# Optimization experiments

Measured on AMD Instinct MI355X. Metric: run time of the kernel, lower is better.

## Reference

```python
import jax, jax.numpy as jnp
import numpy as np
from jax import lax


def extract_patches(x, kh, kw, sh, sw):
    # x: [B,H,W,C] -> [B,oh,ow,kh,kw,C], same element order as tf.image.extract_patches
    B, H, W, C = x.shape
    oh = (H - kh) // sh + 1
    ow = (W - kw) // sw + 1
    rows = jnp.arange(oh)[:, None] * sh + jnp.arange(kh)[None, :]  # [oh,kh]
    cols = jnp.arange(ow)[:, None] * sw + jnp.arange(kw)[None, :]  # [ow,kw]
    p = x[:, rows]            # [B,oh,kh,W,C]
    p = p[:, :, :, cols]      # [B,oh,kh,ow,kw,C]
    return jnp.transpose(p, (0, 1, 3, 2, 4, 5))  # [B,oh,ow,kh,kw,C]


def fastgrnn(x, W, U, bg, bu, zeta, nu):
    # FastGRNN: z=sigmoid(Wx+Uh+bg); c=tanh(Wx+Uh+bu); h'=z*h+(sig(zeta)*(1-z)+sig(nu))*c
    # x: [N,T,D] -> final hidden [N,H]
    wx = jnp.einsum('ntd,dh->nth', x, W)  # precompute input projection
    z_gate = jax.nn.sigmoid(zeta)
    n_gate = jax.nn.sigmoid(nu)

    def step(h, wx_t):
        pre = wx_t + h @ U
        z = jax.nn.sigmoid(pre + bg)
        c = jnp.tanh(pre + bu)
        h_new = z * h + (z_gate * (1.0 - z) + n_gate) * c
        return h_new, None

    h0 = jnp.zeros((x.shape[0], W.shape[1]), x.dtype)
    hT, _ = lax.scan(step, h0, jnp.swapaxes(wx, 0, 1))  # scan over T
    return hT


def rnnpool_forward(inputs, W1, U1, bg1, bu1, zeta1, nu1,
                    W2, U2, bg2, bu2, zeta2, nu2, kh, kw, sh, sw):
    B, H, Wd, C = inputs.shape
    oh = (H - kh) // sh + 1
    ow = (Wd - kw) // sw + 1
    patches = extract_patches(inputs, kh, kw, sh, sw)          # [B,oh,ow,kh,kw,C]
    N = B * oh * ow
    p = patches.reshape(N, kh, kw, C)

    u = W1.shape[1]
    # row-wise: rnn1 scans along cols within each row
    x = p.reshape(N * kh, kw, C)
    h = fastgrnn(x, W1, U1, bg1, bu1, zeta1, nu1).reshape(N, kh, u)
    o21 = fastgrnn(h, W2, U2, bg2, bu2, zeta2, nu2)
    o22 = fastgrnn(h[:, ::-1, :], W2, U2, bg2, bu2, zeta2, nu2)

    # col-wise: transpose patch, rnn1 scans along rows within each col
    xc = jnp.transpose(p, (0, 2, 1, 3)).reshape(N * kw, kh, C)
    hc = fastgrnn(xc, W1, U1, bg1, bu1, zeta1, nu1).reshape(N, kw, u)
    o23 = fastgrnn(hc, W2, U2, bg2, bu2, zeta2, nu2)
    o24 = fastgrnn(hc[:, ::-1, :], W2, U2, bg2, bu2, zeta2, nu2)

    out = jnp.concatenate([o21, o22, o23, o24], axis=1)        # [N, 4*hOut]
    return out.reshape(B, oh, ow, -1)


def setup_inputs() -> dict:
    key = jax.random.key(0)
    ks = jax.random.split(key, 9)
    C, u, hout = 16, 8, 16  # in-channels, rnn1 hidden, rnn2 hidden (out_channel//4)
    s = 0.1
    inp = {
        'inputs': jax.random.normal(ks[0], (32, 112, 112, C), jnp.float32),
        'W1': jax.random.normal(ks[1], (C, u), jnp.float32) * s,
        'U1': jax.random.normal(ks[2], (u, u), jnp.float32) * s,
        'bg1': jnp.ones((u,), jnp.float32),
        'bu1': jnp.ones((u,), jnp.float32),
        'zeta1': jnp.float32(100.0),
        'nu1': jnp.float32(-100.0),
        'W2': jax.random.normal(ks[3], (u, hout), jnp.float32) * s,
        'U2': jax.random.normal(ks[4], (hout, hout), jnp.float32) * s,
        'bg2': jnp.ones((hout,), jnp.float32),
        'bu2': jnp.ones((hout,), jnp.float32),
        'zeta2': jnp.float32(100.0),
        'nu2': jnp.float32(-100.0),
        'kh': 8, 'kw': 8, 'sh': 4, 'sw': 4,
    }
    return inp


def reference(inputs, W1, U1, bg1, bu1, zeta1, nu1,
              W2, U2, bg2, bu2, zeta2, nu2, kh, kw, sh, sw):
    return rnnpool_forward(inputs, W1, U1, bg1, bu1, zeta1, nu1,
                           W2, U2, bg2, bu2, zeta2, nu2, kh, kw, sh, sw)
```

## Files before the change

kernel.cpp:

```cpp
#include <hip/hip_runtime.h>

#define PPB 4

typedef float v2f __attribute__((ext_vector_type(2)));

__device__ __forceinline__ float frcp(float x) { return __builtin_amdgcn_rcpf(x); }

__device__ __forceinline__ v2f vfma2(v2f a, v2f b, v2f c) {
#if __has_builtin(__builtin_elementwise_fma)
  return __builtin_elementwise_fma(a, b, c);
#else
  v2f d; d.x = fmaf(a.x, b.x, c.x); d.y = fmaf(a.y, b.y, c.y); return d;
#endif
}
__device__ __forceinline__ v2f bc(float x) { v2f p; p.x = x; p.y = x; return p; }

__device__ __forceinline__ v2f gate2(v2f pre, v2f h, v2f bgB, v2f KB, v2f nzgB,
                                     v2f AB, bool first) {
  v2f a = pre + bgB;
  v2f s; s.x = __expf(-a.x); s.y = __expf(-a.y);
  v2f one = bc(1.f);
  v2f zd = s + one;
  v2f z; z.x = frcp(zd.x); z.y = frcp(zd.y);
  v2f u = (s * s) * KB;
  v2f cd = u + one;
  v2f cr; cr.x = frcp(cd.x); cr.y = frcp(cd.y);
  v2f cc = vfma2(cr, bc(2.f), bc(-1.f));
  v2f m = vfma2(z, nzgB, AB);
  v2f mc = m * cc;
  return first ? mc : vfma2(z, h, mc);
}

__global__ __launch_bounds__(256) void l1_kernel(
    const float* __restrict__ inp, const float* __restrict__ W1,
    const float* __restrict__ U1, const float* __restrict__ bg1,
    const float* __restrict__ bu1, const float* __restrict__ zeta1,
    const float* __restrict__ nu1, float* __restrict__ hrowg,
    float* __restrict__ hcolg) {
  constexpr int NP = 6048;
  constexpr int SAs = 68;
  constexpr int SH = 18;

  __shared__ float w1s[128];
  __shared__ float wxs[PPB][16 * SAs];
  __shared__ v2f hp[PPB][7 * SH + 8];

  const int tid = threadIdx.x, wv = tid >> 6, lane = tid & 63;
  const int widx = blockIdx.x * PPB + wv;

  if (tid < 32) ((float4*)w1s)[tid] = ((const float4*)W1)[tid];
  __syncthreads();

  const bool isrow = widx < NP;
  const int v = isrow ? widx : widx - NP;
  const int b = v / 189;
  const int rem = v % 189;
  const int k = rem / 27;
  const int t27 = rem % 27;

  const int rr = lane >> 3, cc = lane & 7;
  const int ay = isrow ? (k * 16 + rr) : (t27 * 4 + rr);
  const int ax = isrow ? (t27 * 4 + cc) : (k * 16 + cc);
  const int by = isrow ? (ay + 8) : ay;
  const int bx = isrow ? ax : (ax + 8);

  {
    const float* pA = inp + ((size_t)(b * 112 + ay) * 112 + ax) * 16;
    const float* pB = inp + ((size_t)(b * 112 + by) * 112 + bx) * 16;
    float4 A0 = ((const float4*)pA)[0], A1 = ((const float4*)pA)[1],
           A2 = ((const float4*)pA)[2], A3 = ((const float4*)pA)[3];
    float4 B0 = ((const float4*)pB)[0], B1 = ((const float4*)pB)[1],
           B2 = ((const float4*)pB)[2], B3 = ((const float4*)pB)[3];
    float xA[16] = {A0.x, A0.y, A0.z, A0.w, A1.x, A1.y, A1.z, A1.w,
                    A2.x, A2.y, A2.z, A2.w, A3.x, A3.y, A3.z, A3.w};
    float xB[16] = {B0.x, B0.y, B0.z, B0.w, B1.x, B1.y, B1.z, B1.w,
                    B2.x, B2.y, B2.z, B2.w, B3.x, B3.y, B3.z, B3.w};
    float aA[8] = {0, 0, 0, 0, 0, 0, 0, 0};
    float aB[8] = {0, 0, 0, 0, 0, 0, 0, 0};
#pragma unroll
    for (int ci = 0; ci < 16; ++ci) {
      float4 wL = *(const float4*)&w1s[ci * 8];
      float4 wH = *(const float4*)&w1s[ci * 8 + 4];
      aA[0] = fmaf(xA[ci], wL.x, aA[0]); aA[1] = fmaf(xA[ci], wL.y, aA[1]);
      aA[2] = fmaf(xA[ci], wL.z, aA[2]); aA[3] = fmaf(xA[ci], wL.w, aA[3]);
      aA[4] = fmaf(xA[ci], wH.x, aA[4]); aA[5] = fmaf(xA[ci], wH.y, aA[5]);
      aA[6] = fmaf(xA[ci], wH.z, aA[6]); aA[7] = fmaf(xA[ci], wH.w, aA[7]);
      aB[0] = fmaf(xB[ci], wL.x, aB[0]); aB[1] = fmaf(xB[ci], wL.y, aB[1]);
      aB[2] = fmaf(xB[ci], wL.z, aB[2]); aB[3] = fmaf(xB[ci], wL.w, aB[3]);
      aB[4] = fmaf(xB[ci], wH.x, aB[4]); aB[5] = fmaf(xB[ci], wH.y, aB[5]);
      aB[6] = fmaf(xB[ci], wH.z, aB[6]); aB[7] = fmaf(xB[ci], wH.w, aB[7]);
    }
    const int a0 = isrow ? rr : cc;
    const int b0 = isrow ? cc : rr;
    float* wdA = &wxs[wv][a0 * SAs + b0 * 8];
    float* wdB = &wxs[wv][(a0 + 8) * SAs + b0 * 8];
    ((float4*)wdA)[0] = float4{aA[0], aA[1], aA[2], aA[3]};
    ((float4*)wdA)[1] = float4{aA[4], aA[5], aA[6], aA[7]};
    ((float4*)wdB)[0] = float4{aB[0], aB[1], aB[2], aB[3]};
    ((float4*)wdB)[1] = float4{aB[4], aB[5], aB[6], aB[7]};
  }
  __builtin_amdgcn_wave_barrier();

  const int seq = rr, hid = cc;
  v2f u1b[8];
#pragma unroll
  for (int i = 0; i < 8; ++i) u1b[i] = bc(U1[i * 8 + hid]);
  const float bg1v = bg1[hid], bu1v = bu1[hid];
  const float zg1 = frcp(1.f + __expf(-zeta1[0]));
  const float ng1 = frcp(1.f + __expf(-nu1[0]));
  const v2f bgB = bc(bg1v);
  const v2f KB = bc(__expf(2.f * (bg1v - bu1v)));
  const v2f nzgB = bc(-zg1);
  const v2f AB = bc(zg1 + ng1);

  v2f* hq = &hp[wv][0];
  v2f h; h.x = 0.f; h.y = 0.f;
  {
    v2f pre;
    pre.x = wxs[wv][seq * SAs + hid];
    pre.y = wxs[wv][(seq + 8) * SAs + hid];
    h = gate2(pre, h, bgB, KB, nzgB, AB, true);
    hq[seq * SH + hid] = h;
  }
  __builtin_amdgcn_wave_barrier();
#pragma unroll
  for (int t = 1; t < 8; ++t) {
    v2f q = hq[seq * SH + 0] * u1b[0];
#pragma unroll
    for (int i = 1; i < 8; ++i) q = vfma2(hq[seq * SH + i], u1b[i], q);
    v2f pre;
    pre.x = wxs[wv][seq * SAs + t * 8 + hid];
    pre.y = wxs[wv][(seq + 8) * SAs + t * 8 + hid];
    pre = pre + q;
    h = gate2(pre, h, bgB, KB, nzgB, AB, false);
    hq[seq * SH + hid] = h;
    __builtin_amdgcn_wave_barrier();
  }

  const size_t obase = (((size_t)(b * 27 + t27) * 112) + k * 16 + seq) * 8 + hid;
  float* dst = isrow ? hrowg : hcolg;
  dst[obase] = h.x;
  dst[obase + 64] = h.y;
}

__global__ __launch_bounds__(256) void l2_kernel(
    const float* __restrict__ hrowg, const float* __restrict__ hcolg,
    const float* __restrict__ W2, const float* __restrict__ U2,
    const float* __restrict__ bg2, const float* __restrict__ bu2,
    const float* __restrict__ zeta2, const float* __restrict__ nu2,
    float* __restrict__ out) {
  constexpr int GST = 18;
  __shared__ v2f hbI[PPB][128];
  __shared__ v2f h2I[PPB][3 * GST + 16];

  const int tid = threadIdx.x, wv = tid >> 6, lane = tid & 63;
  const int w = blockIdx.x * PPB + wv;
  const int n0 = 2 * w, n1 = n0 + 1;

  {
    const int p = lane >> 5, half = (lane >> 4) & 1, idx = lane & 15;
    const int pn = p ? n1 : n0;
    const int pw = pn % 27;
    const int qq = pn / 27;
    const int ph = qq % 27, bb = qq / 27;
    const float* src = half ? &hcolg[(((size_t)(bb * 27 + ph)) * 112 + pw * 4) * 8]
                            : &hrowg[(((size_t)(bb * 27 + pw)) * 112 + ph * 4) * 8];
    float4 val = ((const float4*)src)[idx];
    float* base = (float*)&hbI[wv][half * 64 + idx * 4];
    base[0 + p] = val.x;
    base[2 + p] = val.y;
    base[4 + p] = val.z;
    base[6 + p] = val.w;
  }
  __builtin_amdgcn_wave_barrier();

  const int g = lane >> 4, j = lane & 15;
  v2f w2b[8], u2b[16];
#pragma unroll
  for (int d = 0; d < 8; ++d) w2b[d] = bc(W2[d * 16 + j]);
#pragma unroll
  for (int i = 0; i < 16; ++i) u2b[i] = bc(U2[i * 16 + j]);
  const float bg2v = bg2[j], bu2v = bu2[j];
  const float zg2 = frcp(1.f + __expf(-zeta2[0]));
  const float ng2 = frcp(1.f + __expf(-nu2[0]));
  const v2f bgB = bc(bg2v);
  const v2f KB = bc(__expf(2.f * (bg2v - bu2v)));
  const v2f nzgB = bc(-zg2);
  const v2f AB = bc(zg2 + ng2);

  const v2f* hsrc = &hbI[wv][(g >> 1) * 64];
  v2f* h2q = &h2I[wv][g * GST];

  v2f h2; h2.x = 0.f; h2.y = 0.f;
  {
    const int tt = (g & 1) ? 7 : 0;
    v2f p = hsrc[tt * 8 + 0] * w2b[0];
#pragma unroll
    for (int d = 1; d < 8; ++d) p = vfma2(hsrc[tt * 8 + d], w2b[d], p);
    h2 = gate2(p, h2, bgB, KB, nzgB, AB, true);
    h2q[j] = h2;
  }
  __builtin_amdgcn_wave_barrier();
#pragma unroll
  for (int t = 1; t < 8; ++t) {
    const int tt = (g & 1) ? (7 - t) : t;
    v2f p = hsrc[tt * 8 + 0] * w2b[0];
#pragma unroll
    for (int d = 1; d < 8; ++d) p = vfma2(hsrc[tt * 8 + d], w2b[d], p);
    v2f q = h2q[0] * u2b[0];
#pragma unroll
    for (int i = 1; i < 16; ++i) q = vfma2(h2q[i], u2b[i], q);
    v2f pre = p + q;
    h2 = gate2(pre, h2, bgB, KB, nzgB, AB, false);
    if (t < 7) {
      h2q[j] = h2;
      __builtin_amdgcn_wave_barrier();
    }
  }

  out[(size_t)n0 * 64 + lane] = h2.x;
  out[(size_t)n1 * 64 + lane] = h2.y;
}

extern "C" void kernel_launch(void* const* d_in, const int* in_sizes, int n_in,
                              void* d_out, int out_size, void* d_ws, size_t ws_size,
                              hipStream_t stream) {
  const float* inp   = (const float*)d_in[0];
  const float* W1    = (const float*)d_in[1];
  const float* U1    = (const float*)d_in[2];
  const float* bg1   = (const float*)d_in[3];
  const float* bu1   = (const float*)d_in[4];
  const float* zeta1 = (const float*)d_in[5];
  const float* nu1   = (const float*)d_in[6];
  const float* W2    = (const float*)d_in[7];
  const float* U2    = (const float*)d_in[8];
  const float* bg2   = (const float*)d_in[9];
  const float* bu2   = (const float*)d_in[10];
  const float* zeta2 = (const float*)d_in[11];
  const float* nu2   = (const float*)d_in[12];
  float* out = (float*)d_out;

  const size_t HSZ = (size_t)32 * 27 * 112 * 8;
  float* hrowg = (float*)d_ws;
  float* hcolg = hrowg + HSZ;

  l1_kernel<<<dim3(3024), dim3(256), 0, stream>>>(
      inp, W1, U1, bg1, bu1, zeta1, nu1, hrowg, hcolg);
  l2_kernel<<<dim3(2916), dim3(256), 0, stream>>>(
      hrowg, hcolg, W2, U2, bg2, bu2, zeta2, nu2, out);
}
```

Baseline: 37.66 us.

## Use DPP row rotations for layer-2 recurrence, one patch per wave

```diff
diff --git a/kernel.cpp b/kernel.cpp
--- a/kernel.cpp
+++ b/kernel.cpp
@@ -14,6 +14,12 @@
 #endif
 }
 __device__ __forceinline__ v2f bc(float x) { v2f p; p.x = x; p.y = x; return p; }
+
+template <int K>
+__device__ __forceinline__ float rotr(float x) {
+  return __int_as_float(
+      __builtin_amdgcn_mov_dpp(__float_as_int(x), 0x120 + K, 0xf, 0xf, true));
+}
 
 __device__ __forceinline__ v2f gate2(v2f pre, v2f h, v2f bgB, v2f KB, v2f nzgB,
                                      v2f AB, bool first) {
@@ -75,29 +81,26 @@
                     A2.x, A2.y, A2.z, A2.w, A3.x, A3.y, A3.z, A3.w};
     float xB[16] = {B0.x, B0.y, B0.z, B0.w, B1.x, B1.y, B1.z, B1.w,
                     B2.x, B2.y, B2.z, B2.w, B3.x, B3.y, B3.z, B3.w};
-    float aA[8] = {0, 0, 0, 0, 0, 0, 0, 0};
-    float aB[8] = {0, 0, 0, 0, 0, 0, 0, 0};
+    v2f aA0 = bc(0.f), aA1 = bc(0.f), aA2 = bc(0.f), aA3 = bc(0.f);
+    v2f aB0 = bc(0.f), aB1 = bc(0.f), aB2 = bc(0.f), aB3 = bc(0.f);
 #pragma unroll
     for (int ci = 0; ci < 16; ++ci) {
-      float4 wL = *(const float4*)&w1s[ci * 8];
-      float4 wH = *(const float4*)&w1s[ci * 8 + 4];
-      aA[0] = fmaf(xA[ci], wL.x, aA[0]); aA[1] = fmaf(xA[ci], wL.y, aA[1]);
-      aA[2] = fmaf(xA[ci], wL.z, aA[2]); aA[3] = fmaf(xA[ci], wL.w, aA[3]);
-      aA[4] = fmaf(xA[ci], wH.x, aA[4]); aA[5] = fmaf(xA[ci], wH.y, aA[5]);
-      aA[6] = fmaf(xA[ci], wH.z, aA[6]); aA[7] = fmaf(xA[ci], wH.w, aA[7]);
-      aB[0] = fmaf(xB[ci], wL.x, aB[0]); aB[1] = fmaf(xB[ci], wL.y, aB[1]);
-      aB[2] = fmaf(xB[ci], wL.z, aB[2]); aB[3] = fmaf(xB[ci], wL.w, aB[3]);
-      aB[4] = fmaf(xB[ci], wH.x, aB[4]); aB[5] = fmaf(xB[ci], wH.y, aB[5]);
-      aB[6] = fmaf(xB[ci], wH.z, aB[6]); aB[7] = fmaf(xB[ci], wH.w, aB[7]);
+      const v2f* wr = (const v2f*)&w1s[ci * 8];
+      v2f w0 = wr[0], w1 = wr[1], w2 = wr[2], w3 = wr[3];
+      v2f xa = bc(xA[ci]), xb = bc(xB[ci]);
+      aA0 = vfma2(xa, w0, aA0); aA1 = vfma2(xa, w1, aA1);
+      aA2 = vfma2(xa, w2, aA2); aA3 = vfma2(xa, w3, aA3);
+      aB0 = vfma2(xb, w0, aB0); aB1 = vfma2(xb, w1, aB1);
+      aB2 = vfma2(xb, w2, aB2); aB3 = vfma2(xb, w3, aB3);
     }
     const int a0 = isrow ? rr : cc;
     const int b0 = isrow ? cc : rr;
     float* wdA = &wxs[wv][a0 * SAs + b0 * 8];
     float* wdB = &wxs[wv][(a0 + 8) * SAs + b0 * 8];
-    ((float4*)wdA)[0] = float4{aA[0], aA[1], aA[2], aA[3]};
-    ((float4*)wdA)[1] = float4{aA[4], aA[5], aA[6], aA[7]};
-    ((float4*)wdB)[0] = float4{aB[0], aB[1], aB[2], aB[3]};
-    ((float4*)wdB)[1] = float4{aB[4], aB[5], aB[6], aB[7]};
+    ((float4*)wdA)[0] = float4{aA0.x, aA0.y, aA1.x, aA1.y};
+    ((float4*)wdA)[1] = float4{aA2.x, aA2.y, aA3.x, aA3.y};
+    ((float4*)wdB)[0] = float4{aB0.x, aB0.y, aB1.x, aB1.y};
+    ((float4*)wdB)[1] = float4{aB2.x, aB2.y, aB3.x, aB3.y};
   }
   __builtin_amdgcn_wave_barrier();
 
@@ -114,7 +117,7 @@
   const v2f AB = bc(zg1 + ng1);
 
   v2f* hq = &hp[wv][0];
-  v2f h; h.x = 0.f; h.y = 0.f;
+  v2f h = bc(0.f);
   {
     v2f pre;
     pre.x = wxs[wv][seq * SAs + hid];
@@ -125,9 +128,16 @@
   __builtin_amdgcn_wave_barrier();
 #pragma unroll
   for (int t = 1; t < 8; ++t) {
-    v2f q = hq[seq * SH + 0] * u1b[0];
-#pragma unroll
-    for (int i = 1; i < 8; ++i) q = vfma2(hq[seq * SH + i], u1b[i], q);
+    const float4* hr4 = (const float4*)&hq[seq * SH];
+    float4 f0 = hr4[0], f1 = hr4[1], f2 = hr4[2], f3 = hr4[3];
+    v2f q = v2f{f0.x, f0.y} * u1b[0];
+    q = vfma2(v2f{f0.z, f0.w}, u1b[1], q);
+    q = vfma2(v2f{f1.x, f1.y}, u1b[2], q);
+    q = vfma2(v2f{f1.z, f1.w}, u1b[3], q);
+    q = vfma2(v2f{f2.x, f2.y}, u1b[4], q);
+    q = vfma2(v2f{f2.z, f2.w}, u1b[5], q);
+    q = vfma2(v2f{f3.x, f3.y}, u1b[6], q);
+    q = vfma2(v2f{f3.z, f3.w}, u1b[7], q);
     v2f pre;
     pre.x = wxs[wv][seq * SAs + t * 8 + hid];
     pre.y = wxs[wv][(seq + 8) * SAs + t * 8 + hid];
@@ -149,77 +159,72 @@
     const float* __restrict__ bg2, const float* __restrict__ bu2,
     const float* __restrict__ zeta2, const float* __restrict__ nu2,
     float* __restrict__ out) {
-  constexpr int GST = 18;
-  __shared__ v2f hbI[PPB][128];
-  __shared__ v2f h2I[PPB][3 * GST + 16];
-
   const int tid = threadIdx.x, wv = tid >> 6, lane = tid & 63;
-  const int w = blockIdx.x * PPB + wv;
-  const int n0 = 2 * w, n1 = n0 + 1;
-
-  {
-    const int p = lane >> 5, half = (lane >> 4) & 1, idx = lane & 15;
-    const int pn = p ? n1 : n0;
-    const int pw = pn % 27;
-    const int qq = pn / 27;
-    const int ph = qq % 27, bb = qq / 27;
-    const float* src = half ? &hcolg[(((size_t)(bb * 27 + ph)) * 112 + pw * 4) * 8]
-                            : &hrowg[(((size_t)(bb * 27 + pw)) * 112 + ph * 4) * 8];
-    float4 val = ((const float4*)src)[idx];
-    float* base = (float*)&hbI[wv][half * 64 + idx * 4];
-    base[0 + p] = val.x;
-    base[2 + p] = val.y;
-    base[4 + p] = val.z;
-    base[6 + p] = val.w;
-  }
-  __builtin_amdgcn_wave_barrier();
-
   const int g = lane >> 4, j = lane & 15;
-  v2f w2b[8], u2b[16];
-#pragma unroll
-  for (int d = 0; d < 8; ++d) w2b[d] = bc(W2[d * 16 + j]);
-#pragma unroll
-  for (int i = 0; i < 16; ++i) u2b[i] = bc(U2[i * 16 + j]);
-  const float bg2v = bg2[j], bu2v = bu2[j];
-  const float zg2 = frcp(1.f + __expf(-zeta2[0]));
-  const float ng2 = frcp(1.f + __expf(-nu2[0]));
-  const v2f bgB = bc(bg2v);
-  const v2f KB = bc(__expf(2.f * (bg2v - bu2v)));
-  const v2f nzgB = bc(-zg2);
-  const v2f AB = bc(zg2 + ng2);
-
-  const v2f* hsrc = &hbI[wv][(g >> 1) * 64];
-  v2f* h2q = &h2I[wv][g * GST];
-
-  v2f h2; h2.x = 0.f; h2.y = 0.f;
-  {
-    const int tt = (g & 1) ? 7 : 0;
-    v2f p = hsrc[tt * 8 + 0] * w2b[0];
-#pragma unroll
-    for (int d = 1; d < 8; ++d) p = vfma2(hsrc[tt * 8 + d], w2b[d], p);
-    h2 = gate2(p, h2, bgB, KB, nzgB, AB, true);
-    h2q[j] = h2;
-  }
-  __builtin_amdgcn_wave_barrier();
-#pragma unroll
-  for (int t = 1; t < 8; ++t) {
-    const int tt = (g & 1) ? (7 - t) : t;
-    v2f p = hsrc[tt * 8 + 0] * w2b[0];
-#pragma unroll
-    for (int d = 1; d < 8; ++d) p = vfma2(hsrc[tt * 8 + d], w2b[d], p);
-    v2f q = h2q[0] * u2b[0];
-#pragma unroll
-    for (int i = 1; i < 16; ++i) q = vfma2(h2q[i], u2b[i], q);
-    v2f pre = p + q;
-    h2 = gate2(pre, h2, bgB, KB, nzgB, AB, false);
-    if (t < 7) {
-      h2q[j] = h2;
-      __builtin_amdgcn_wave_barrier();
+  const int n = blockIdx.x * 4 + wv;
+  const int pw = n % 27;
+  const int q = n / 27;
+  const int ph = q % 27, b = q / 27;
+  const int rev = g & 1;
+
+  const float* hs = (g < 2)
+      ? &hrowg[((size_t)(b * 27 + pw) * 112 + ph * 4) * 8]
+      : &hcolg[((size_t)(b * 27 + ph) * 112 + pw * 4) * 8];
+
+  float w2c[8];
+#pragma unroll
+  for (int d = 0; d < 8; ++d) w2c[d] = W2[d * 16 + j];
+  float u2r[16];
+#pragma unroll
+  for (int k = 0; k < 16; ++k) u2r[k] = U2[((j - k) & 15) * 16 + j];
+  const float bgv = bg2[j];
+  const float Kc = __expf(2.f * (bg2[j] - bu2[j]));
+  const float zg = frcp(1.f + __expf(-zeta2[0]));
+  const float ng = frcp(1.f + __expf(-nu2[0]));
+  const float A = zg + ng;
+
+  float h2 = 0.f;
+#pragma unroll
+  for (int t = 0; t < 8; ++t) {
+    const int tt = rev ? (7 - t) : t;
+    const float4* rp = (const float4*)(hs + tt * 8);
+    float4 r0 = rp[0], r1 = rp[1];
+    float pa = r0.x * w2c[0], pb = r0.y * w2c[1];
+    pa = fmaf(r0.z, w2c[2], pa);
+    pb = fmaf(r0.w, w2c[3], pb);
+    pa = fmaf(r1.x, w2c[4], pa);
+    pb = fmaf(r1.y, w2c[5], pb);
+    pa = fmaf(r1.z, w2c[6], pa);
+    pb = fmaf(r1.w, w2c[7], pb);
+    float pre = pa + pb;
+    if (t > 0) {
+      float a0 = h2 * u2r[0];
+      float a1 = rotr<1>(h2) * u2r[1];
+      a0 = fmaf(rotr<2>(h2), u2r[2], a0);
+      a1 = fmaf(rotr<3>(h2), u2r[3], a1);
+      a0 = fmaf(rotr<4>(h2), u2r[4], a0);
+      a1 = fmaf(rotr<5>(h2), u2r[5], a1);
+      a0 = fmaf(rotr<6>(h2), u2r[6], a0);
+      a1 = fmaf(rotr<7>(h2), u2r[7], a1);
+      a0 = fmaf(rotr<8>(h2), u2r[8], a0);
+      a1 = fmaf(rotr<9>(h2), u2r[9], a1);
+      a0 = fmaf(rotr<10>(h2), u2r[10], a0);
+      a1 = fmaf(rotr<11>(h2), u2r[11], a1);
+      a0 = fmaf(rotr<12>(h2), u2r[12], a0);
+      a1 = fmaf(rotr<13>(h2), u2r[13], a1);
+      a0 = fmaf(rotr<14>(h2), u2r[14], a0);
+      a1 = fmaf(rotr<15>(h2), u2r[15], a1);
+      pre += a0 + a1;
     }
-  }
-
-  out[(size_t)n0 * 64 + lane] = h2.x;
-  out[(size_t)n1 * 64 + lane] = h2.y;
+    float s = __expf(-(pre + bgv));
+    float z = frcp(1.f + s);
+    float u = s * s * Kc;
+    float c = fmaf(2.f, frcp(1.f + u), -1.f);
+    float m = fmaf(-zg, z, A);
+    h2 = fmaf(z, h2, m * c);
+  }
+
+  out[(size_t)n * 64 + lane] = h2;
 }
 
 extern "C" void kernel_launch(void* const* d_in, const int* in_sizes, int n_in,
@@ -246,6 +251,6 @@
 
   l1_kernel<<<dim3(3024), dim3(256), 0, stream>>>(
       inp, W1, U1, bg1, bu1, zeta1, nu1, hrowg, hcolg);
-  l2_kernel<<<dim3(2916), dim3(256), 0, stream>>>(
+  l2_kernel<<<dim3(5832), dim3(256), 0, stream>>>(
       hrowg, hcolg, W2, U2, bg2, bu2, zeta2, nu2, out);
 }
```

Measured after the change: 51.78 us. +37.5%, slower.

## Exchange recurrent hidden state via DPP lane shuffles instead of LDS

Applied to the files above, without the earlier changes.

```diff
diff --git a/kernel.cpp b/kernel.cpp
--- a/kernel.cpp
+++ b/kernel.cpp
@@ -14,6 +14,22 @@
 #endif
 }
 __device__ __forceinline__ v2f bc(float x) { v2f p; p.x = x; p.y = x; return p; }
+
+template <int CTRL>
+__device__ __forceinline__ float dppf(float x) {
+  return __int_as_float(
+      __builtin_amdgcn_mov_dpp(__float_as_int(x), CTRL, 0xf, 0xf, true));
+}
+template <int P>
+__device__ __forceinline__ v2f qbcast(v2f v) {
+  constexpr int ctrl = P * 0x55;
+  v2f r; r.x = dppf<ctrl>(v.x); r.y = dppf<ctrl>(v.y); return r;
+}
+template <int K>
+__device__ __forceinline__ v2f rot16(v2f v) {
+  constexpr int ctrl = 0x120 + K;
+  v2f r; r.x = dppf<ctrl>(v.x); r.y = dppf<ctrl>(v.y); return r;
+}
 
 __device__ __forceinline__ v2f gate2(v2f pre, v2f h, v2f bgB, v2f KB, v2f nzgB,
                                      v2f AB, bool first) {
@@ -38,12 +54,11 @@
     const float* __restrict__ nu1, float* __restrict__ hrowg,
     float* __restrict__ hcolg) {
   constexpr int NP = 6048;
-  constexpr int SAs = 68;
-  constexpr int SH = 18;
+  constexpr int TS = 132;
+  constexpr int TILE1 = 8 * TS;
 
   __shared__ float w1s[128];
-  __shared__ float wxs[PPB][16 * SAs];
-  __shared__ v2f hp[PPB][7 * SH + 8];
+  __shared__ float wxs[PPB][2 * TILE1 + 16];
 
   const int tid = threadIdx.x, wv = tid >> 6, lane = tid & 63;
   const int widx = blockIdx.x * PPB + wv;
@@ -75,72 +90,67 @@
                     A2.x, A2.y, A2.z, A2.w, A3.x, A3.y, A3.z, A3.w};
     float xB[16] = {B0.x, B0.y, B0.z, B0.w, B1.x, B1.y, B1.z, B1.w,
                     B2.x, B2.y, B2.z, B2.w, B3.x, B3.y, B3.z, B3.w};
-    float aA[8] = {0, 0, 0, 0, 0, 0, 0, 0};
-    float aB[8] = {0, 0, 0, 0, 0, 0, 0, 0};
+    v2f aA0 = bc(0.f), aA1 = bc(0.f), aA2 = bc(0.f), aA3 = bc(0.f);
+    v2f aB0 = bc(0.f), aB1 = bc(0.f), aB2 = bc(0.f), aB3 = bc(0.f);
 #pragma unroll
     for (int ci = 0; ci < 16; ++ci) {
-      float4 wL = *(const float4*)&w1s[ci * 8];
-      float4 wH = *(const float4*)&w1s[ci * 8 + 4];
-      aA[0] = fmaf(xA[ci], wL.x, aA[0]); aA[1] = fmaf(xA[ci], wL.y, aA[1]);
-      aA[2] = fmaf(xA[ci], wL.z, aA[2]); aA[3] = fmaf(xA[ci], wL.w, aA[3]);
-      aA[4] = fmaf(xA[ci], wH.x, aA[4]); aA[5] = fmaf(xA[ci], wH.y, aA[5]);
-      aA[6] = fmaf(xA[ci], wH.z, aA[6]); aA[7] = fmaf(xA[ci], wH.w, aA[7]);
-      aB[0] = fmaf(xB[ci], wL.x, aB[0]); aB[1] = fmaf(xB[ci], wL.y, aB[1]);
-      aB[2] = fmaf(xB[ci], wL.z, aB[2]); aB[3] = fmaf(xB[ci], wL.w, aB[3]);
-      aB[4] = fmaf(xB[ci], wH.x, aB[4]); aB[5] = fmaf(xB[ci], wH.y, aB[5]);
-      aB[6] = fmaf(xB[ci], wH.z, aB[6]); aB[7] = fmaf(xB[ci], wH.w, aB[7]);
+      const v2f* wr = (const v2f*)&w1s[ci * 8];
+      v2f w0 = wr[0], w1 = wr[1], w2 = wr[2], w3 = wr[3];
+      v2f xa = bc(xA[ci]), xb = bc(xB[ci]);
+      aA0 = vfma2(xa, w0, aA0); aA1 = vfma2(xa, w1, aA1);
+      aA2 = vfma2(xa, w2, aA2); aA3 = vfma2(xa, w3, aA3);
+      aB0 = vfma2(xb, w0, aB0); aB1 = vfma2(xb, w1, aB1);
+      aB2 = vfma2(xb, w2, aB2); aB3 = vfma2(xb, w3, aB3);
     }
-    const int a0 = isrow ? rr : cc;
-    const int b0 = isrow ? cc : rr;
-    float* wdA = &wxs[wv][a0 * SAs + b0 * 8];
-    float* wdB = &wxs[wv][(a0 + 8) * SAs + b0 * 8];
-    ((float4*)wdA)[0] = float4{aA[0], aA[1], aA[2], aA[3]};
-    ((float4*)wdA)[1] = float4{aA[4], aA[5], aA[6], aA[7]};
-    ((float4*)wdB)[0] = float4{aB[0], aB[1], aB[2], aB[3]};
-    ((float4*)wdB)[1] = float4{aB[4], aB[5], aB[6], aB[7]};
+    const int tA = isrow ? cc : rr;
+    const int qA = isrow ? rr : cc;
+    float* wdA = &wxs[wv][tA * TS + qA * 8];
+    float* wdB = wdA + TILE1;
+    ((float4*)wdA)[0] = float4{aA0.x, aA0.y, aA1.x, aA1.y};
+    ((float4*)wdA)[1] = float4{aA2.x, aA2.y, aA3.x, aA3.y};
+    ((float4*)wdB)[0] = float4{aB0.x, aB0.y, aB1.x, aB1.y};
+    ((float4*)wdB)[1] = float4{aB2.x, aB2.y, aB3.x, aB3.y};
   }
   __builtin_amdgcn_wave_barrier();
 
-  const int seq = rr, hid = cc;
-  v2f u1b[8];
-#pragma unroll
-  for (int i = 0; i < 8; ++i) u1b[i] = bc(U1[i * 8 + hid]);
-  const float bg1v = bg1[hid], bu1v = bu1[hid];
+  const int q4 = lane >> 2, sub = lane & 3;
+  v2f wxv[8];
+  {
+    const float* base = &wxs[wv][(q4 >> 3) * TILE1 + (q4 & 7) * 8 + 2 * sub];
+#pragma unroll
+    for (int t = 0; t < 8; ++t) wxv[t] = *(const v2f*)(base + t * TS);
+  }
+
+  v2f u1q[8];
+#pragma unroll
+  for (int i = 0; i < 8; ++i) u1q[i] = *(const v2f*)&U1[i * 8 + 2 * sub];
+  const v2f bgB = *(const v2f*)&bg1[2 * sub];
+  const v2f buB = *(const v2f*)&bu1[2 * sub];
   const float zg1 = frcp(1.f + __expf(-zeta1[0]));
   const float ng1 = frcp(1.f + __expf(-nu1[0]));
-  const v2f bgB = bc(bg1v);
-  const v2f KB = bc(__expf(2.f * (bg1v - bu1v)));
+  v2f KB; KB.x = __expf(2.f * (bgB.x - buB.x)); KB.y = __expf(2.f * (bgB.y - buB.y));
   const v2f nzgB = bc(-zg1);
   const v2f AB = bc(zg1 + ng1);
 
-  v2f* hq = &hp[wv][0];
-  v2f h; h.x = 0.f; h.y = 0.f;
-  {
-    v2f pre;
-    pre.x = wxs[wv][seq * SAs + hid];
-    pre.y = wxs[wv][(seq + 8) * SAs + hid];
-    h = gate2(pre, h, bgB, KB, nzgB, AB, true);
-    hq[seq * SH + hid] = h;
-  }
-  __builtin_amdgcn_wave_barrier();
+  v2f h = gate2(wxv[0], bc(0.f), bgB, KB, nzgB, AB, true);
 #pragma unroll
   for (int t = 1; t < 8; ++t) {
-    v2f q = hq[seq * SH + 0] * u1b[0];
-#pragma unroll
-    for (int i = 1; i < 8; ++i) q = vfma2(hq[seq * SH + i], u1b[i], q);
-    v2f pre;
-    pre.x = wxs[wv][seq * SAs + t * 8 + hid];
-    pre.y = wxs[wv][(seq + 8) * SAs + t * 8 + hid];
-    pre = pre + q;
-    h = gate2(pre, h, bgB, KB, nzgB, AB, false);
-    hq[seq * SH + hid] = h;
-    __builtin_amdgcn_wave_barrier();
-  }
-
-  const size_t obase = (((size_t)(b * 27 + t27) * 112) + k * 16 + seq) * 8 + hid;
-  float* dst = isrow ? hrowg : hcolg;
-  dst[obase] = h.x;
-  dst[obase + 64] = h.y;
+    v2f h0 = qbcast<0>(h), h1 = qbcast<1>(h), h2_ = qbcast<2>(h), h3 = qbcast<3>(h);
+    v2f q = bc(h0.x) * u1q[0];
+    q = vfma2(bc(h0.y), u1q[1], q);
+    q = vfma2(bc(h1.x), u1q[2], q);
+    q = vfma2(bc(h1.y), u1q[3], q);
+    q = vfma2(bc(h2_.x), u1q[4], q);
+    q = vfma2(bc(h2_.y), u1q[5], q);
+    q = vfma2(bc(h3.x), u1q[6], q);
+    q = vfma2(bc(h3.y), u1q[7], q);
+    h = gate2(wxv[t] + q, h, bgB, KB, nzgB, AB, false);
+  }
+
+  float* dst = (isrow ? hrowg : hcolg) +
+               (((size_t)(b * 27 + t27) * 112) + k * 16 + q4) * 8 + 2 * sub;
+  dst[0] = h.x;
+  dst[1] = h.y;
 }
 
 __global__ __launch_bounds__(256) void l2_kernel(
@@ -149,9 +159,9 @@
     const float* __restrict__ bg2, const float* __restrict__ bu2,
     const float* __restrict__ zeta2, const float* __restrict__ nu2,
     float* __restrict__ out) {
-  constexpr int GST = 18;
+  constexpr int WHT = 18;
   __shared__ v2f hbI[PPB][128];
-  __shared__ v2f h2I[PPB][3 * GST + 16];
+  __shared__ v2f whb[PPB][2 * 8 * WHT];
 
   const int tid = threadIdx.x, wv = tid >> 6, lane = tid & 63;
   const int w = blockIdx.x * PPB + wv;
@@ -175,11 +185,12 @@
   __builtin_amdgcn_wave_barrier();
 
   const int g = lane >> 4, j = lane & 15;
-  v2f w2b[8], u2b[16];
+  v2f w2b[8];
 #pragma unroll
   for (int d = 0; d < 8; ++d) w2b[d] = bc(W2[d * 16 + j]);
-#pragma unroll
-  for (int i = 0; i < 16; ++i) u2b[i] = bc(U2[i * 16 + j]);
+  v2f u2r[16];
+#pragma unroll
+  for (int kk = 0; kk < 16; ++kk) u2r[kk] = bc(U2[((j - kk) & 15) * 16 + j]);
   const float bg2v = bg2[j], bu2v = bu2[j];
   const float zg2 = frcp(1.f + __expf(-zeta2[0]));
   const float ng2 = frcp(1.f + __expf(-nu2[0]));
@@ -188,34 +199,53 @@
   const v2f nzgB = bc(-zg2);
   const v2f AB = bc(zg2 + ng2);
 
-  const v2f* hsrc = &hbI[wv][(g >> 1) * 64];
-  v2f* h2q = &h2I[wv][g * GST];
-
-  v2f h2; h2.x = 0.f; h2.y = 0.f;
-  {
-    const int tt = (g & 1) ? 7 : 0;
-    v2f p = hsrc[tt * 8 + 0] * w2b[0];
-#pragma unroll
-    for (int d = 1; d < 8; ++d) p = vfma2(hsrc[tt * 8 + d], w2b[d], p);
-    h2 = gate2(p, h2, bgB, KB, nzgB, AB, true);
-    h2q[j] = h2;
+  const int src = g >> 1;
+
+  {
+    const v2f* hb = &hbI[wv][src * 64];
+    const int t0 = (g & 1) * 4;
+#pragma unroll
+    for (int i = 0; i < 4; ++i) {
+      const int t = t0 + i;
+      const v2f* hr = &hb[t * 8];
+      v2f p = hr[0] * w2b[0];
+#pragma unroll
+      for (int d = 1; d < 8; ++d) p = vfma2(hr[d], w2b[d], p);
+      whb[wv][(src * 8 + t) * WHT + j] = p;
+    }
   }
   __builtin_amdgcn_wave_barrier();
+
+  v2f whv[8];
+  {
+    const v2f* whsrc = &whb[wv][src * 8 * WHT];
+#pragma unroll
+    for (int t = 0; t < 8; ++t) {
+      const int tt = (g & 1) ? (7 - t) : t;
+      whv[t] = whsrc[tt * WHT + j];
+    }
+  }
+
+  v2f h2 = gate2(whv[0], bc(0.f), bgB, KB, nzgB, AB, true);
 #pragma unroll
   for (int t = 1; t < 8; ++t) {
-    const int tt = (g & 1) ? (7 - t) : t;
-    v2f p = hsrc[tt * 8 + 0] * w2b[0];
-#pragma unroll
-    for (int d = 1; d < 8; ++d) p = vfma2(hsrc[tt * 8 + d], w2b[d], p);
-    v2f q = h2q[0] * u2b[0];
-#pragma unroll
-    for (int i = 1; i < 16; ++i) q = vfma2(h2q[i], u2b[i], q);
-    v2f pre = p + q;
-    h2 = gate2(pre, h2, bgB, KB, nzgB, AB, false);
-    if (t < 7) {
-      h2q[j] = h2;
-      __builtin_amdgcn_wave_barrier();
-    }
+    v2f q = h2 * u2r[0];
+    q = vfma2(rot16<1>(h2), u2r[1], q);
+    q = vfma2(rot16<2>(h2), u2r[2], q);
+    q = vfma2(rot16<3>(h2), u2r[3], q);
+    q = vfma2(rot16<4>(h2), u2r[4], q);
+    q = vfma2(rot16<5>(h2), u2r[5], q);
+    q = vfma2(rot16<6>(h2), u2r[6], q);
+    q = vfma2(rot16<7>(h2), u2r[7], q);
+    q = vfma2(rot16<8>(h2), u2r[8], q);
+    q = vfma2(rot16<9>(h2), u2r[9], q);
+    q = vfma2(rot16<10>(h2), u2r[10], q);
+    q = vfma2(rot16<11>(h2), u2r[11], q);
+    q = vfma2(rot16<12>(h2), u2r[12], q);
+    q = vfma2(rot16<13>(h2), u2r[13], q);
+    q = vfma2(rot16<14>(h2), u2r[14], q);
+    q = vfma2(rot16<15>(h2), u2r[15], q);
+    h2 = gate2(whv[t] + q, h2, bgB, KB, nzgB, AB, false);
   }
 
   out[(size_t)n0 * 64 + lane] = h2.x;
```

After: 38.43 us. +2.1%, slower.
